# Kernel tuning notes

Measured on AMD Instinct MI355X. Metric: run time of the kernel, lower is better.

The kernel has to match this reference:

```python
import jax, jax.numpy as jnp
import numpy as np

N_NODES = 50000
N_EDGES = 800000
F_IN = 128
HIDDEN = 128
N_CLASSES = 40


def setup_inputs() -> dict:
    key = jax.random.key(0)
    ks = jax.random.split(key, 8)
    x = jax.random.normal(ks[0], (N_NODES, F_IN), dtype=jnp.float32)
    edge_index = jax.random.randint(ks[1], (2, N_EDGES), 0, N_NODES, dtype=jnp.int32)
    s_in = 1.0 / np.sqrt(F_IN)
    s_h = 1.0 / np.sqrt(HIDDEN)
    W1_l = jax.random.normal(ks[2], (F_IN, HIDDEN), jnp.float32) * s_in
    W1_r = jax.random.normal(ks[3], (F_IN, HIDDEN), jnp.float32) * s_in
    b1 = jnp.zeros((HIDDEN,), jnp.float32)
    W2_l = jax.random.normal(ks[4], (HIDDEN, N_CLASSES), jnp.float32) * s_h
    W2_r = jax.random.normal(ks[5], (HIDDEN, N_CLASSES), jnp.float32) * s_h
    b2 = jnp.zeros((N_CLASSES,), jnp.float32)
    return {"x": x, "edge_index": edge_index, "W1_l": W1_l, "W1_r": W1_r,
            "b1": b1, "W2_l": W2_l, "W2_r": W2_r, "b2": b2}


def _sage_conv(x, src, dst, W_l, W_r, b):
    # mean-aggregate neighbor features at dst, then linear transform + root weight
    msg = x[src]                                                  # [E, d] gather
    agg = jax.ops.segment_sum(msg, dst, num_segments=N_NODES)     # [N, d] scatter-add
    deg = jax.ops.segment_sum(jnp.ones((src.shape[0],), x.dtype), dst,
                              num_segments=N_NODES)
    agg = agg / jnp.maximum(deg, 1.0)[:, None]                    # mean aggregation
    return agg @ W_l + x @ W_r + b


def reference(x, edge_index, W1_l, W1_r, b1, W2_l, W2_r, b2):
    src, dst = edge_index[0], edge_index[1]
    h = jax.nn.relu(_sage_conv(x, src, dst, W1_l, W1_r, b1))
    # F.dropout(p=0.5, training=self.training) -> identity in eval mode
    out = jax.nn.relu(_sage_conv(h, src, dst, W2_l, W2_r, b2))
    return jax.nn.log_softmax(out, axis=-1)
```

## Files before the change

### kernel.cpp

```cpp
#include <hip/hip_runtime.h>

#define N_NODES 50000
#define N_EDGES 800000
#define F_IN 128
#define HIDDEN 128
#define N_CLASSES 40

#define NBUCKET 391
#define BUCKET_CAP 4096
#define BINA_CHUNK 2048
#define BINA_NBLK 391
#define PREP_ITEMS (N_NODES * 32 + 128 * 256 + 80 * 128)
#define PREP_NBLK (PREP_ITEMS / 256)

#define OFF_RS     0
#define OFF_BCNT   50004
#define OFF_INVDEG 100004
#define OFF_SRCS   150004
#define OFF_XB     950004
#define OFF_BINS   7350004
#define OFF_PB     7350004
#define OFF_Q      8350004
#define OFF_WT1    10550004
#define OFF_WT2    10566388

typedef short bf16x8 __attribute__((ext_vector_type(8)));
typedef float f32x4 __attribute__((ext_vector_type(4)));
typedef unsigned short u16x8 __attribute__((ext_vector_type(8)));

static __device__ __forceinline__ unsigned short f2bf(float f) {
  unsigned int u = __builtin_bit_cast(unsigned int, f);
  u = (u + 0x7fffu + ((u >> 16) & 1u)) >> 16;
  return (unsigned short)u;
}
static __device__ __forceinline__ float bf2f(unsigned short s) {
  unsigned int u = ((unsigned int)s) << 16;
  return __builtin_bit_cast(float, u);
}

__global__ __launch_bounds__(256) void k_binA_prep(
    const int* __restrict__ src, const int* __restrict__ dst,
    int* __restrict__ bcnt, int* __restrict__ bins,
    const float* __restrict__ x, const float* __restrict__ W1l,
    const float* __restrict__ W1r, const float* __restrict__ W2l,
    const float* __restrict__ W2r, unsigned short* __restrict__ xb,
    unsigned short* __restrict__ Wt1, unsigned short* __restrict__ Wt2) {
  if (blockIdx.x >= BINA_NBLK) {
    int idx = (blockIdx.x - BINA_NBLK) * 256 + threadIdx.x;
    if (idx < N_NODES * 32) {
      int row = idx >> 5, c4 = (idx & 31) << 2;
      const float4 v = *(const float4*)(x + (size_t)row * F_IN + c4);
      ushort4 o;
      o.x = f2bf(v.x); o.y = f2bf(v.y); o.z = f2bf(v.z); o.w = f2bf(v.w);
      *(ushort4*)(xb + (size_t)row * 128 + c4) = o;
      return;
    }
    idx -= N_NODES * 32;
    if (idx < 128 * 256) {
      int n = idx >> 8, k = idx & 255;
      float v = (k < 128) ? W1l[(size_t)k * 128 + n]
                          : W1r[(size_t)(k - 128) * 128 + n];
      Wt1[(size_t)n * 256 + k] = f2bf(v);
    } else if (idx < 128 * 256 + 80 * 128) {
      int j = idx - 128 * 256;
      int n = j >> 7, k = j & 127;
      float v = (n < 40) ? W2l[(size_t)k * 40 + n]
                         : W2r[(size_t)k * 40 + (n - 40)];
      Wt2[(size_t)n * 128 + k] = f2bf(v);
    }
    return;
  }
  __shared__ int cnt[NBUCKET];
  __shared__ int excl[NBUCKET];
  __shared__ int cursor[NBUCKET];
  __shared__ int bbase[NBUCKET];
  __shared__ int sc[256];
  __shared__ int stage[BINA_CHUNK];
  __shared__ unsigned short bkt[BINA_CHUNK];
  int t = threadIdx.x;
  int e0 = blockIdx.x * BINA_CHUNK;
  int ne = N_EDGES - e0;
  if (ne > BINA_CHUNK) ne = BINA_CHUNK;
  for (int i = t; i < NBUCKET; i += 256) cnt[i] = 0;
  __syncthreads();
  for (int i = t; i < ne; i += 256) atomicAdd(&cnt[dst[e0 + i] >> 7], 1);
  __syncthreads();
  int a = (2 * t < NBUCKET) ? cnt[2 * t] : 0;
  int b2_ = (2 * t + 1 < NBUCKET) ? cnt[2 * t + 1] : 0;
  int s = a + b2_;
  sc[t] = s;
  __syncthreads();
  for (int off = 1; off < 256; off <<= 1) {
    int add = (t >= off) ? sc[t - off] : 0;
    __syncthreads();
    sc[t] += add;
    __syncthreads();
  }
  int pbase = sc[t] - s;
  if (2 * t < NBUCKET) { excl[2 * t] = pbase; cursor[2 * t] = pbase; }
  if (2 * t + 1 < NBUCKET) {
    excl[2 * t + 1] = pbase + a;
    cursor[2 * t + 1] = pbase + a;
  }
  for (int i = t; i < NBUCKET; i += 256)
    bbase[i] = atomicAdd(&bcnt[i], cnt[i]);
  __syncthreads();
  for (int i = t; i < ne; i += 256) {
    int d = dst[e0 + i];
    int sv = src[e0 + i];
    int b = d >> 7;
    int pos = atomicAdd(&cursor[b], 1);
    stage[pos] = ((d & 127) << 16) | sv;
    bkt[pos] = (unsigned short)b;
  }
  __syncthreads();
  for (int i = t; i < ne; i += 256) {
    int b = bkt[i];
    bins[(size_t)b * BUCKET_CAP + bbase[b] + (i - excl[b])] = stage[i];
  }
}

__global__ __launch_bounds__(256) void k_binB(
    const int* __restrict__ bcnt, const int* __restrict__ bins,
    int* __restrict__ rs, int* __restrict__ srcs,
    float* __restrict__ invdeg) {
  __shared__ int sc[256];
  __shared__ int hist[128];
  __shared__ int cursor[128];
  int b = blockIdx.x;
  int t = threadIdx.x;
  int v = 0;
  if (t < b) v += bcnt[t];
  if (t + 256 < b) v += bcnt[t + 256];
  sc[t] = v;
  __syncthreads();
  for (int off = 128; off; off >>= 1) {
    if (t < off) sc[t] += sc[t + off];
    __syncthreads();
  }
  int base = sc[0];
  int cnt = bcnt[b];
  const int* bb = bins + (size_t)b * BUCKET_CAP;
  if (t < 128) hist[t] = 0;
  __syncthreads();
  for (int i = t; i < cnt; i += 256) atomicAdd(&hist[bb[i] >> 16], 1);
  __syncthreads();
  int c = (t < 128) ? hist[t] : 0;
  sc[t] = c;
  __syncthreads();
  for (int off = 1; off < 128; off <<= 1) {
    int add = (t >= off) ? sc[t - off] : 0;
    __syncthreads();
    sc[t] += add;
    __syncthreads();
  }
  int lexcl = sc[t] - c;
  int node = b * 128 + t;
  if (t < 128 && node < N_NODES) {
    rs[node] = base + lexcl;
    invdeg[node] = 1.0f / (float)(c > 1 ? c : 1);
  }
  if (b == 0 && t == 0) rs[N_NODES] = N_EDGES;
  if (t < 128) cursor[t] = lexcl;
  __syncthreads();
  for (int i = t; i < cnt; i += 256) {
    int v2 = bb[i];
    int pos = atomicAdd(&cursor[v2 >> 16], 1);
    srcs[base + pos] = v2 & 0xFFFF;
  }
}

__global__ __launch_bounds__(512) void k_fused(
    const unsigned short* __restrict__ xb, const int* __restrict__ rs,
    const int* __restrict__ srcs, const float* __restrict__ invdeg,
    const unsigned short* __restrict__ Wt1, const unsigned short* __restrict__ Wt2,
    const float* __restrict__ b1, const float* __restrict__ b2,
    unsigned short* __restrict__ pb, float* __restrict__ q) {
  __shared__ unsigned short as[64 * 264];
  unsigned short* hs = as;
  int w = threadIdx.x >> 6, lane = threadIdx.x & 63;
  int t = threadIdx.x;
  int row0 = blockIdx.x * 64;

  for (int chunk = t; chunk < 64 * 16; chunk += 512) {
    int lrow = chunk >> 4, c8 = (chunk & 15) * 8;
    int grow = row0 + lrow;
    if (grow >= N_NODES) grow = N_NODES - 1;
    u16x8 v = *(const u16x8*)(xb + (size_t)grow * 128 + c8);
    *(u16x8*)(as + lrow * 264 + 128 + c8) = v;
  }

  int slot = lane >> 3, li = lane & 7;
  for (int j = 0; j < 8; j++) {
    int lrow = w * 8 + j;
    int node = row0 + lrow;
    int beg = 0, end = 0;
    if (node < N_NODES) { beg = rs[node]; end = rs[node + 1]; }
    float acc[16];
#pragma unroll
    for (int k = 0; k < 16; k++) acc[k] = 0.f;
    int i = beg + slot;
    for (; i + 8 < end; i += 16) {
      int s0 = srcs[i], s1 = srcs[i + 8];
      const unsigned short* rp0 = xb + (size_t)s0 * 128 + li * 8;
      const unsigned short* rp1 = xb + (size_t)s1 * 128 + li * 8;
      u16x8 a0 = *(const u16x8*)rp0;
      u16x8 a1 = *(const u16x8*)(rp0 + 64);
      u16x8 c0 = *(const u16x8*)rp1;
      u16x8 c1 = *(const u16x8*)(rp1 + 64);
#pragma unroll
      for (int k = 0; k < 8; k++) {
        acc[k] += bf2f(a0[k]) + bf2f(c0[k]);
        acc[8 + k] += bf2f(a1[k]) + bf2f(c1[k]);
      }
    }
    if (i < end) {
      int s0 = srcs[i];
      const unsigned short* rp0 = xb + (size_t)s0 * 128 + li * 8;
      u16x8 a0 = *(const u16x8*)rp0;
      u16x8 a1 = *(const u16x8*)(rp0 + 64);
#pragma unroll
      for (int k = 0; k < 8; k++) {
        acc[k] += bf2f(a0[k]);
        acc[8 + k] += bf2f(a1[k]);
      }
    }
#pragma unroll
    for (int off = 8; off <= 32; off <<= 1)
#pragma unroll
      for (int k = 0; k < 16; k++) acc[k] += __shfl_xor(acc[k], off, 64);
    if (slot == 0) {
      int nidx = (node < N_NODES) ? node : 0;
      float inv = invdeg[nidx];
      u16x8 o0, o1;
#pragma unroll
      for (int k = 0; k < 8; k++) {
        o0[k] = f2bf(acc[k] * inv);
        o1[k] = f2bf(acc[8 + k] * inv);
      }
      *(u16x8*)(as + lrow * 264 + li * 8) = o0;
      *(u16x8*)(as + lrow * 264 + 64 + li * 8) = o1;
    }
  }
  __syncthreads();

  int r = lane & 15, quad = lane >> 4;
  const unsigned short* Bp = Wt1 + (size_t)(w * 16 + r) * 256 + quad * 8;
  f32x4 acc1[4];
#pragma unroll
  for (int rt = 0; rt < 4; rt++) acc1[rt] = (f32x4){0.f, 0.f, 0.f, 0.f};
#pragma unroll
  for (int k0 = 0; k0 < 256; k0 += 32) {
    bf16x8 bv = *(const bf16x8*)(Bp + k0);
#pragma unroll
    for (int rt = 0; rt < 4; rt++) {
      bf16x8 av = *(const bf16x8*)(as + (rt * 16 + r) * 264 + quad * 8 + k0);
      acc1[rt] = __builtin_amdgcn_mfma_f32_16x16x32_bf16(av, bv, acc1[rt], 0, 0, 0);
    }
  }
  __syncthreads();
  {
    int col = w * 16 + r;
    float bias = b1[col];
#pragma unroll
    for (int rt = 0; rt < 4; rt++)
#pragma unroll
      for (int reg = 0; reg < 4; reg++)
        hs[(rt * 16 + quad * 4 + reg) * 132 + col] =
            f2bf(fmaxf(acc1[rt][reg] + bias, 0.f));
  }
  __syncthreads();

  int rt2 = w >> 1, ng = w & 1;
  int nbeg = ng ? 3 : 0;
  int ncnt = ng ? 2 : 3;
  const unsigned short* hrow = hs + (rt2 * 16 + r) * 132 + quad * 8;
  const unsigned short* Bp2 = Wt2 + (size_t)(nbeg * 16 + r) * 128 + quad * 8;
  f32x4 acc2[3];
#pragma unroll
  for (int j = 0; j < 3; j++) acc2[j] = (f32x4){0.f, 0.f, 0.f, 0.f};
#pragma unroll
  for (int k0 = 0; k0 < 128; k0 += 32) {
    ushort4 h0 = *(const ushort4*)(hrow + k0);
    ushort4 h1 = *(const ushort4*)(hrow + k0 + 4);
    bf16x8 af;
    af[0] = (short)h0.x; af[1] = (short)h0.y; af[2] = (short)h0.z; af[3] = (short)h0.w;
    af[4] = (short)h1.x; af[5] = (short)h1.y; af[6] = (short)h1.z; af[7] = (short)h1.w;
#pragma unroll
    for (int j = 0; j < 3; j++) {
      if (j < ncnt) {
        bf16x8 bv = *(const bf16x8*)(Bp2 + (size_t)j * 16 * 128 + k0);
        acc2[j] = __builtin_amdgcn_mfma_f32_16x16x32_bf16(af, bv, acc2[j], 0, 0, 0);
      }
    }
  }
  int crow0 = row0 + rt2 * 16 + quad * 4;
#pragma unroll
  for (int j = 0; j < 3; j++) {
    if (j < ncnt) {
      int col = (nbeg + j) * 16 + r;
#pragma unroll
      for (int reg = 0; reg < 4; reg++) {
        int row = crow0 + reg;
        if (row < N_NODES) {
          float v = acc2[j][reg];
          if (col < N_CLASSES)
            pb[(size_t)row * 40 + col] = f2bf(v);
          else
            q[(size_t)row * N_CLASSES + (col - N_CLASSES)] = v + b2[col - N_CLASSES];
        }
      }
    }
  }
}

__global__ __launch_bounds__(256) void k_final(
    const unsigned short* __restrict__ pb, const float* __restrict__ q,
    const int* __restrict__ rs, const int* __restrict__ srcs,
    const float* __restrict__ invdeg, float* __restrict__ out) {
  int node = blockIdx.x * 4 + (threadIdx.x >> 6);
  int lane = threadIdx.x & 63;
  int slot = lane >> 3, li = lane & 7;
  if (node >= N_NODES) return;
  bool valid = li < 5;
  int beg = rs[node], end = rs[node + 1];
  float acc[8];
#pragma unroll
  for (int j = 0; j < 8; j++) acc[j] = 0.f;
  int i = beg + slot;
  for (; i + 8 < end; i += 16) {
    int s0 = srcs[i], s1 = srcs[i + 8];
    if (valid) {
      u16x8 v0 = *(const u16x8*)(pb + (size_t)s0 * 40 + li * 8);
      u16x8 v1 = *(const u16x8*)(pb + (size_t)s1 * 40 + li * 8);
#pragma unroll
      for (int j = 0; j < 8; j++) acc[j] += bf2f(v0[j]) + bf2f(v1[j]);
    }
  }
  if (i < end) {
    int s0 = srcs[i];
    if (valid) {
      u16x8 v0 = *(const u16x8*)(pb + (size_t)s0 * 40 + li * 8);
#pragma unroll
      for (int j = 0; j < 8; j++) acc[j] += bf2f(v0[j]);
    }
  }
#pragma unroll
  for (int off = 8; off <= 32; off <<= 1)
#pragma unroll
    for (int j = 0; j < 8; j++) acc[j] += __shfl_xor(acc[j], off, 64);
  float inv = invdeg[node];
  float v[8];
  float m = -1e30f;
  if (valid) {
    const float* qr = q + (size_t)node * N_CLASSES + li * 8;
    float4 q0 = *(const float4*)qr;
    float4 q1 = *(const float4*)(qr + 4);
    v[0] = fmaxf(acc[0] * inv + q0.x, 0.f);
    v[1] = fmaxf(acc[1] * inv + q0.y, 0.f);
    v[2] = fmaxf(acc[2] * inv + q0.z, 0.f);
    v[3] = fmaxf(acc[3] * inv + q0.w, 0.f);
    v[4] = fmaxf(acc[4] * inv + q1.x, 0.f);
    v[5] = fmaxf(acc[5] * inv + q1.y, 0.f);
    v[6] = fmaxf(acc[6] * inv + q1.z, 0.f);
    v[7] = fmaxf(acc[7] * inv + q1.w, 0.f);
#pragma unroll
    for (int j = 0; j < 8; j++) m = fmaxf(m, v[j]);
  }
#pragma unroll
  for (int off = 1; off <= 4; off <<= 1) m = fmaxf(m, __shfl_xor(m, off, 8));
  float ssum = 0.f;
  if (valid) {
#pragma unroll
    for (int j = 0; j < 8; j++) ssum += __expf(v[j] - m);
  }
#pragma unroll
  for (int off = 1; off <= 4; off <<= 1) ssum += __shfl_xor(ssum, off, 8);
  float lse = __logf(ssum) + m;
  if (slot == 0 && valid) {
    float* orow = out + (size_t)node * N_CLASSES + li * 8;
    *(float4*)orow = make_float4(v[0] - lse, v[1] - lse, v[2] - lse, v[3] - lse);
    *(float4*)(orow + 4) =
        make_float4(v[4] - lse, v[5] - lse, v[6] - lse, v[7] - lse);
  }
}

extern "C" void kernel_launch(void* const* d_in, const int* in_sizes, int n_in,
                              void* d_out, int out_size, void* d_ws,
                              size_t ws_size, hipStream_t stream) {
  const float* x   = (const float*)d_in[0];
  const int*   ei  = (const int*)d_in[1];
  const int*   src = ei;
  const int*   dst = ei + N_EDGES;
  const float* W1l = (const float*)d_in[2];
  const float* W1r = (const float*)d_in[3];
  const float* b1  = (const float*)d_in[4];
  const float* W2l = (const float*)d_in[5];
  const float* W2r = (const float*)d_in[6];
  const float* b2  = (const float*)d_in[7];
  float* out = (float*)d_out;

  float* wsf = (float*)d_ws;
  int*   rs     = (int*)wsf + OFF_RS;
  int*   bcnt   = (int*)wsf + OFF_BCNT;
  float* invdeg = wsf + OFF_INVDEG;
  int*   srcs   = (int*)wsf + OFF_SRCS;
  unsigned short* xb  = (unsigned short*)(wsf + OFF_XB);
  unsigned short* pb  = (unsigned short*)(wsf + OFF_PB);
  unsigned short* Wt1 = (unsigned short*)(wsf + OFF_WT1);
  unsigned short* Wt2 = (unsigned short*)(wsf + OFF_WT2);
  int*   bins   = (int*)wsf + OFF_BINS;
  float* q = wsf + OFF_Q;

  hipMemsetAsync(bcnt, 0, NBUCKET * sizeof(int), stream);

  k_binA_prep<<<BINA_NBLK + PREP_NBLK, 256, 0, stream>>>(
      src, dst, bcnt, bins, x, W1l, W1r, W2l, W2r, xb, Wt1, Wt2);
  k_binB<<<NBUCKET, 256, 0, stream>>>(bcnt, bins, rs, srcs, invdeg);
  k_fused<<<(N_NODES + 63) / 64, 512, 0, stream>>>(
      xb, rs, srcs, invdeg, Wt1, Wt2, b1, b2, pb, q);
  k_final<<<(N_NODES + 3) / 4, 256, 0, stream>>>(pb, q, rs, srcs, invdeg, out);
}
```

Baseline: 207.5 us.

## Store bf16 features in column-chunked layout for cache-local neighbor gathers

```diff
diff --git a/kernel.cpp b/kernel.cpp
--- a/kernel.cpp
+++ b/kernel.cpp
@@ -52,7 +52,8 @@
       const float4 v = *(const float4*)(x + (size_t)row * F_IN + c4);
       ushort4 o;
       o.x = f2bf(v.x); o.y = f2bf(v.y); o.z = f2bf(v.z); o.w = f2bf(v.w);
-      *(ushort4*)(xb + (size_t)row * 128 + c4) = o;
+      int cc = c4 >> 5, wi = c4 & 31;
+      *(ushort4*)(xb + ((size_t)cc * N_NODES + row) * 32 + wi) = o;
       return;
     }
     idx -= N_NODES * 32;
@@ -183,63 +184,51 @@
   int row0 = blockIdx.x * 64;
 
   for (int chunk = t; chunk < 64 * 16; chunk += 512) {
-    int lrow = chunk >> 4, c8 = (chunk & 15) * 8;
+    int lrow = chunk >> 4, p = chunk & 15;
+    int cc = p >> 2, wi = (p & 3) * 8;
     int grow = row0 + lrow;
     if (grow >= N_NODES) grow = N_NODES - 1;
-    u16x8 v = *(const u16x8*)(xb + (size_t)grow * 128 + c8);
-    *(u16x8*)(as + lrow * 264 + 128 + c8) = v;
-  }
-
-  int slot = lane >> 3, li = lane & 7;
-  for (int j = 0; j < 8; j++) {
-    int lrow = w * 8 + j;
-    int node = row0 + lrow;
-    int beg = 0, end = 0;
-    if (node < N_NODES) { beg = rs[node]; end = rs[node + 1]; }
-    float acc[16];
-#pragma unroll
-    for (int k = 0; k < 16; k++) acc[k] = 0.f;
-    int i = beg + slot;
-    for (; i + 8 < end; i += 16) {
-      int s0 = srcs[i], s1 = srcs[i + 8];
-      const unsigned short* rp0 = xb + (size_t)s0 * 128 + li * 8;
-      const unsigned short* rp1 = xb + (size_t)s1 * 128 + li * 8;
-      u16x8 a0 = *(const u16x8*)rp0;
-      u16x8 a1 = *(const u16x8*)(rp0 + 64);
-      u16x8 c0 = *(const u16x8*)rp1;
-      u16x8 c1 = *(const u16x8*)(rp1 + 64);
-#pragma unroll
-      for (int k = 0; k < 8; k++) {
-        acc[k] += bf2f(a0[k]) + bf2f(c0[k]);
-        acc[8 + k] += bf2f(a1[k]) + bf2f(c1[k]);
+    u16x8 v = *(const u16x8*)(xb + ((size_t)cc * N_NODES + grow) * 32 + wi);
+    *(u16x8*)(as + lrow * 264 + 128 + cc * 32 + wi) = v;
+  }
+
+  int slot = lane >> 2, li = lane & 3;
+  for (int cc = 0; cc < 4; cc++) {
+    const unsigned short* xc = xb + (size_t)cc * N_NODES * 32;
+    for (int j = 0; j < 8; j++) {
+      int lrow = w * 8 + j;
+      int node = row0 + lrow;
+      int beg = 0, end = 0;
+      if (node < N_NODES) { beg = rs[node]; end = rs[node + 1]; }
+      float acc[8];
+#pragma unroll
+      for (int k = 0; k < 8; k++) acc[k] = 0.f;
+      int i = beg + slot;
+      for (; i + 16 < end; i += 32) {
+        int s0 = srcs[i], s1 = srcs[i + 16];
+        u16x8 a0 = *(const u16x8*)(xc + (size_t)s0 * 32 + li * 8);
+        u16x8 c0 = *(const u16x8*)(xc + (size_t)s1 * 32 + li * 8);
+#pragma unroll
+        for (int k = 0; k < 8; k++) acc[k] += bf2f(a0[k]) + bf2f(c0[k]);
       }
-    }
-    if (i < end) {
-      int s0 = srcs[i];
-      const unsigned short* rp0 = xb + (size_t)s0 * 128 + li * 8;
-      u16x8 a0 = *(const u16x8*)rp0;
-      u16x8 a1 = *(const u16x8*)(rp0 + 64);
-#pragma unroll
-      for (int k = 0; k < 8; k++) {
-        acc[k] += bf2f(a0[k]);
-        acc[8 + k] += bf2f(a1[k]);
+      if (i < end) {
+        int s0 = srcs[i];
+        u16x8 a0 = *(const u16x8*)(xc + (size_t)s0 * 32 + li * 8);
+#pragma unroll
+        for (int k = 0; k < 8; k++) acc[k] += bf2f(a0[k]);
       }
-    }
-#pragma unroll
-    for (int off = 8; off <= 32; off <<= 1)
-#pragma unroll
-      for (int k = 0; k < 16; k++) acc[k] += __shfl_xor(acc[k], off, 64);
-    if (slot == 0) {
-      int nidx = (node < N_NODES) ? node : 0;
-      float inv = invdeg[nidx];
-      u16x8 o0, o1;
-#pragma unroll
-      for (int k = 0; k < 8; k++) {
-        o0[k] = f2bf(acc[k] * inv);
-        o1[k] = f2bf(acc[8 + k] * inv);
+#pragma unroll
+      for (int off = 4; off <= 32; off <<= 1)
+#pragma unroll
+        for (int k = 0; k < 8; k++) acc[k] += __shfl_xor(acc[k], off, 64);
+      if (slot == 0) {
+        int nidx = (node < N_NODES) ? node : 0;
+        float inv = invdeg[nidx];
+        u16x8 o;
+#pragma unroll
+        for (int k = 0; k < 8; k++) o[k] = f2bf(acc[k] * inv);
+        *(u16x8*)(as + lrow * 264 + cc * 32 + li * 8) = o;
       }
-      *(u16x8*)(as + lrow * 264 + li * 8) = o0;
-      *(u16x8*)(as + lrow * 264 + 64 + li * 8) = o1;
     }
   }
   __syncthreads();
```

Result: slower. 265.6 us (+28.0%).
